# Kernel optimization log

Hardware: AMD Instinct MI355X
Metric: run time of the kernel (lower is better)

The kernel has to match this reference:

```python
import jax, jax.numpy as jnp
import numpy as np

D_MODEL = 512
D_INNER = 1024   # expand=2
D_STATE = 16
D_CONV = 4
DT_RANK = 32     # ceil(d_model/16)
B, L = 2, 2048


def _params(kbase):
    kk = jax.random.split(kbase, 9)
    n = lambda k, s, sc: jax.random.normal(k, s, jnp.float32) * sc
    return dict(
        Win=n(kk[0], (2 * D_INNER, D_MODEL), D_MODEL ** -0.5),
        convw=n(kk[1], (D_INNER, 1, D_CONV), 0.2),
        convb=n(kk[2], (D_INNER,), 0.02),
        Wx=n(kk[3], (DT_RANK + 2 * D_STATE, D_INNER), D_INNER ** -0.5),
        Wdt=n(kk[4], (D_INNER, DT_RANK), DT_RANK ** -0.5),
        dtb=n(kk[5], (D_INNER,), 0.1),
        Alog=n(kk[6], (D_INNER, D_STATE), 0.5),
        Dp=n(kk[7], (D_INNER,), 1.0),
        Wout=n(kk[8], (D_MODEL, D_INNER), D_INNER ** -0.5),
    )


def setup_inputs() -> dict:
    key = jax.random.key(0)
    k0, kf, kr = jax.random.split(key, 3)
    inp = {"hidden_states": jax.random.normal(k0, (B, L, D_MODEL), jnp.float32)}
    for name, v in _params(kf).items():
        inp[name + "_f"] = v
    for name, v in _params(kr).items():
        inp[name + "_r"] = v
    return inp


def _mamba(x, Win, convw, convb, Wx, Wdt, dtb, Alog, Dp, Wout):
    # x: (B, L, D_MODEL)
    Bb = x.shape[0]
    xz = jnp.einsum('bld,ed->ble', x, Win)            # (B, L, 2*D_INNER)
    xs, z = jnp.split(xz, 2, axis=-1)
    # causal depthwise conv over length
    xc = jnp.swapaxes(xs, 1, 2)                       # (B, D_INNER, L)
    xc = jax.lax.conv_general_dilated(
        xc, convw, (1,), [(D_CONV - 1, 0)], feature_group_count=D_INNER)
    xs = jax.nn.silu(jnp.swapaxes(xc + convb[None, :, None], 1, 2))  # (B, L, D_INNER)
    # input-dependent SSM params
    x_dbl = jnp.einsum('bld,ed->ble', xs, Wx)         # (B, L, DT_RANK+2*D_STATE)
    dt = x_dbl[..., :DT_RANK]
    Bm = x_dbl[..., DT_RANK:DT_RANK + D_STATE]        # (B, L, D_STATE)
    Cm = x_dbl[..., DT_RANK + D_STATE:]               # (B, L, D_STATE)
    dt = jax.nn.softplus(jnp.einsum('blr,dr->bld', dt, Wdt) + dtb)   # (B, L, D_INNER)
    A = -jnp.exp(Alog)                                # (D_INNER, D_STATE), strictly negative
    dA = jnp.exp(dt[..., None] * A)                   # (B, L, D_INNER, D_STATE)
    dBu = dt[..., None] * Bm[:, :, None, :] * xs[..., None]

    def step(h, inp):
        dA_t, dBu_t, C_t = inp
        h = dA_t * h + dBu_t                          # (B, D_INNER, D_STATE)
        return h, jnp.einsum('bds,bs->bd', h, C_t)

    h0 = jnp.zeros((Bb, D_INNER, D_STATE), x.dtype)
    _, ys = jax.lax.scan(
        step, h0,
        (jnp.moveaxis(dA, 1, 0), jnp.moveaxis(dBu, 1, 0), jnp.moveaxis(Cm, 1, 0)))
    y = jnp.moveaxis(ys, 0, 1) + xs * Dp              # (B, L, D_INNER)
    y = y * jax.nn.silu(z)                            # gated output
    return jnp.einsum('bld,ed->ble', y, Wout)         # (B, L, D_MODEL)


def reference(hidden_states,
              Win_f, convw_f, convb_f, Wx_f, Wdt_f, dtb_f, Alog_f, Dp_f, Wout_f,
              Win_r, convw_r, convb_r, Wx_r, Wdt_r, dtb_r, Alog_r, Dp_r, Wout_r):
    out_f = _mamba(hidden_states, Win_f, convw_f, convb_f, Wx_f, Wdt_f, dtb_f,
                   Alog_f, Dp_f, Wout_f)
    out_r = _mamba(hidden_states[:, ::-1, :], Win_r, convw_r, convb_r, Wx_r,
                   Wdt_r, dtb_r, Alog_r, Dp_r, Wout_r)[:, ::-1, :]
    return out_f + out_r  # bidirectional_strategy == 'add'
```

## Files before the change

### kernel.cpp

```cpp
#include <hip/hip_runtime.h>
#include <cmath>

#define B_   2
#define L_   2048
#define DM_  512
#define DI_  1024
#define DS_  16
#define DTR_ 32
#define M_   (B_*L_)
#define NC_  64
#define CL_  32
#define KS_  8
#define LOG2E_ 1.44269504088896340736f
#define LN2_   0.69314718055994530942f

typedef __attribute__((ext_vector_type(8))) short short8;
typedef __attribute__((ext_vector_type(4))) float floatx4;

__device__ inline unsigned short f2bf(float f) {
  unsigned u = __float_as_uint(f);
  unsigned r = (u + 0x7fffu + ((u >> 16) & 1u)) >> 16;
  return (unsigned short)r;
}
__device__ inline float bf2f(unsigned short u) {
  return __uint_as_float(((unsigned)u) << 16);
}
__device__ inline unsigned short f2h(float f) {
  _Float16 h = (_Float16)f;
  return *(unsigned short*)&h;
}
__device__ inline float h2f(unsigned short u) {
  _Float16 h = *(_Float16*)&u;
  return (float)h;
}
__device__ inline float fexp2(float x) { return __builtin_amdgcn_exp2f(x); }
__device__ inline float flog2(float x) { return __builtin_amdgcn_logf(x); }

__device__ inline void gload_lds16(const unsigned short* g, unsigned short* l) {
  __builtin_amdgcn_global_load_lds(
      (const __attribute__((address_space(1))) void*)g,
      (__attribute__((address_space(3))) void*)l, 16, 0, 0);
}

__global__ __launch_bounds__(256) void gemm1_mfma_k(
    const unsigned short* __restrict__ A,
    const unsigned short* __restrict__ Wf, const unsigned short* __restrict__ Wr,
    unsigned short* __restrict__ Cf, unsigned short* __restrict__ Cr,
    int M, int N, int K)
{
  __shared__ unsigned short At[128 * 32];
  __shared__ unsigned short Wt[128 * 32];
  const unsigned short* W = blockIdx.z ? Wr : Wf;
  unsigned short* C = blockIdx.z ? Cr : Cf;
  const int tid  = threadIdx.x;
  const int w    = tid >> 6;
  const int lane = tid & 63;
  const int wm   = w >> 1, wn = w & 1;
  const int row0 = blockIdx.y * 128, col0 = blockIdx.x * 128;
  const int lrow  = lane >> 2;
  const int lkoff = (lane & 3) * 8;
  const int fr = lane & 15;
  const int fq = (lane >> 4) * 8;

  floatx4 acc[4][4];
#pragma unroll
  for (int i = 0; i < 4; ++i)
#pragma unroll
    for (int j = 0; j < 4; ++j)
#pragma unroll
      for (int r = 0; r < 4; ++r) acc[i][j][r] = 0.f;

  for (int k0 = 0; k0 < K; k0 += 32) {
#pragma unroll
    for (int j = 0; j < 2; ++j) {
      int r = w * 32 + j * 16;
      gload_lds16(A + (size_t)(row0 + r + lrow) * K + k0 + lkoff, At + r * 32);
      gload_lds16(W + (size_t)(col0 + r + lrow) * K + k0 + lkoff, Wt + r * 32);
    }
    __syncthreads();
    short8 af[4], bf[4];
#pragma unroll
    for (int i = 0; i < 4; ++i) {
      af[i] = *(const short8*)&At[(64 * wm + 16 * i + fr) * 32 + fq];
      bf[i] = *(const short8*)&Wt[(64 * wn + 16 * i + fr) * 32 + fq];
    }
#pragma unroll
    for (int i = 0; i < 4; ++i)
#pragma unroll
      for (int j = 0; j < 4; ++j)
        acc[i][j] = __builtin_amdgcn_mfma_f32_16x16x32_bf16(af[i], bf[j], acc[i][j], 0, 0, 0);
    __syncthreads();
  }
#pragma unroll
  for (int i = 0; i < 4; ++i) {
    int rg = row0 + 64 * wm + 16 * i + ((lane >> 4) << 2);
#pragma unroll
    for (int j = 0; j < 4; ++j) {
      int cg = col0 + 64 * wn + 16 * j + (lane & 15);
#pragma unroll
      for (int r = 0; r < 4; ++r)
        C[(size_t)(rg + r) * N + cg] = f2bf(acc[i][j][r]);
    }
  }
}

__global__ __launch_bounds__(256) void gemm4_fused_k(
    const unsigned short* __restrict__ ybf, const unsigned short* __restrict__ Woutbf,
    const unsigned short* __restrict__ ybr, const unsigned short* __restrict__ Woutbr,
    float* __restrict__ out)
{
  __shared__ unsigned short At[2][64 * 32];
  __shared__ unsigned short Wt[2][64 * 32];
  const int tid  = threadIdx.x;
  const int w    = tid >> 6;
  const int lane = tid & 63;
  const int col0 = blockIdx.x * 64;
  const int row0 = blockIdx.y * 64;
  const int lrow  = lane >> 2;
  const int lkoff = (lane & 3) * 8;
  const int fr = lane & 15;
  const int fq = (lane >> 4) * 8;

  floatx4 acc[4];
#pragma unroll
  for (int j = 0; j < 4; ++j)
#pragma unroll
    for (int r = 0; r < 4; ++r) acc[j][r] = 0.f;

#pragma unroll 1
  for (int src = 0; src < 2; ++src) {
    const unsigned short* A = src ? ybr : ybf;
    const unsigned short* W = src ? Woutbr : Woutbf;
    for (int k0 = 0; k0 < DI_; k0 += 64) {
#pragma unroll
      for (int h = 0; h < 2; ++h) {
        gload_lds16(A + (size_t)(row0 + 16 * w + lrow) * DI_ + k0 + 32 * h + lkoff,
                    At[h] + (16 * w) * 32);
        gload_lds16(W + (size_t)(col0 + 16 * w + lrow) * DI_ + k0 + 32 * h + lkoff,
                    Wt[h] + (16 * w) * 32);
      }
      __syncthreads();
      short8 af[2], bf[2][4];
#pragma unroll
      for (int h = 0; h < 2; ++h) {
        af[h] = *(const short8*)&At[h][(16 * w + fr) * 32 + fq];
#pragma unroll
        for (int j = 0; j < 4; ++j)
          bf[h][j] = *(const short8*)&Wt[h][(16 * j + fr) * 32 + fq];
      }
#pragma unroll
      for (int h = 0; h < 2; ++h)
#pragma unroll
        for (int j = 0; j < 4; ++j)
          acc[j] = __builtin_amdgcn_mfma_f32_16x16x32_bf16(af[h], bf[h][j], acc[j], 0, 0, 0);
      __syncthreads();
    }
  }
  const int rg = row0 + 16 * w + ((lane >> 4) << 2);
#pragma unroll
  for (int j = 0; j < 4; ++j) {
    int cg = col0 + 16 * j + (lane & 15);
#pragma unroll
    for (int r = 0; r < 4; ++r)
      out[(size_t)(rg + r) * DM_ + cg] = acc[j][r];
  }
}

__global__ __launch_bounds__(256) void gemm2_mfma_k(
    const unsigned short* __restrict__ xsbf, const unsigned short* __restrict__ xsbr,
    const unsigned short* __restrict__ Wxbf, const unsigned short* __restrict__ Wxbr,
    float* __restrict__ part)
{
  __shared__ unsigned short At[128 * 32];
  __shared__ unsigned short Wt[64 * 32];
  const int tid  = threadIdx.x;
  const int w    = tid >> 6;
  const int lane = tid & 63;
  const int ks   = blockIdx.x;
  const int row0 = blockIdx.y * 128;
  const int dir  = blockIdx.z;
  const unsigned short* A = dir ? xsbr : xsbf;
  const unsigned short* W = dir ? Wxbr : Wxbf;
  const int kbase = ks * (DI_ / KS_);
  const int lrow  = lane >> 2;
  const int lkoff = (lane & 3) * 8;
  const int fr = lane & 15;
  const int fq = (lane >> 4) * 8;

  floatx4 acc[2][4];
#pragma unroll
  for (int i = 0; i < 2; ++i)
#pragma unroll
    for (int j = 0; j < 4; ++j)
#pragma unroll
      for (int r = 0; r < 4; ++r) acc[i][j][r] = 0.f;

  for (int k0 = 0; k0 < DI_ / KS_; k0 += 32) {
#pragma unroll
    for (int j = 0; j < 2; ++j) {
      int r = w * 32 + j * 16;
      gload_lds16(A + (size_t)(row0 + r + lrow) * DI_ + kbase + k0 + lkoff, At + r * 32);
    }
    {
      int r = w * 16;
      gload_lds16(W + (size_t)(r + lrow) * DI_ + kbase + k0 + lkoff, Wt + r * 32);
    }
    __syncthreads();
    short8 af[2], bf[4];
#pragma unroll
    for (int i = 0; i < 2; ++i)
      af[i] = *(const short8*)&At[(32 * w + 16 * i + fr) * 32 + fq];
#pragma unroll
    for (int j = 0; j < 4; ++j)
      bf[j] = *(const short8*)&Wt[(16 * j + fr) * 32 + fq];
#pragma unroll
    for (int i = 0; i < 2; ++i)
#pragma unroll
      for (int j = 0; j < 4; ++j)
        acc[i][j] = __builtin_amdgcn_mfma_f32_16x16x32_bf16(af[i], bf[j], acc[i][j], 0, 0, 0);
    __syncthreads();
  }
  float* dst = part + (((size_t)dir * KS_ + ks) * M_) * 64;
#pragma unroll
  for (int i = 0; i < 2; ++i) {
    int rg = row0 + 32 * w + 16 * i + ((lane >> 4) << 2);
#pragma unroll
    for (int j = 0; j < 4; ++j) {
      int cg = 16 * j + (lane & 15);
#pragma unroll
      for (int r = 0; r < 4; ++r)
        dst[(size_t)(rg + r) * 64 + cg] = acc[i][j][r];
    }
  }
}

__global__ __launch_bounds__(256) void reduce_part_k(
    const float* __restrict__ part, float* __restrict__ xdf, float* __restrict__ xdr,
    unsigned short* __restrict__ drbf, unsigned short* __restrict__ drbr)
{
  int g = blockIdx.x * 256 + threadIdx.x;
  int n4  = g & 15;
  int m   = (g >> 4) & (M_ - 1);
  int dir = g >> 16;
  const float* p = part + ((size_t)dir * KS_ * M_ + m) * 64 + n4 * 4;
  float4 s = make_float4(0.f, 0.f, 0.f, 0.f);
#pragma unroll
  for (int ks = 0; ks < KS_; ++ks) {
    float4 v = *(const float4*)(p + (size_t)ks * M_ * 64);
    s.x += v.x; s.y += v.y; s.z += v.z; s.w += v.w;
  }
  float* xd = dir ? xdr : xdf;
  *(float4*)(xd + (size_t)m * 64 + n4 * 4) = s;
  if (n4 < 8) {
    unsigned short* dr = dir ? drbr : drbf;
    ushort4 o;
    o.x = f2bf(s.x); o.y = f2bf(s.y); o.z = f2bf(s.z); o.w = f2bf(s.w);
    *(ushort4*)(dr + (size_t)m * 32 + n4 * 4) = o;
  }
}

struct CastArgs {
  const float* src[9];
  unsigned short* dst[9];
  int start[9];
  int n[9];
};

__global__ __launch_bounds__(256) void cast_multi_k(CastArgs a, int total4)
{
  int g = blockIdx.x * 256 + threadIdx.x;
  if (g >= total4) return;
  int e = g * 4;
#pragma unroll 1
  for (int s = 0; s < 9; ++s) {
    if (e < a.start[s] + a.n[s]) {
      int off = e - a.start[s];
      float4 v = *(const float4*)(a.src[s] + off);
      ushort4 o;
      o.x = f2bf(v.x); o.y = f2bf(v.y); o.z = f2bf(v.z); o.w = f2bf(v.w);
      *(ushort4*)(a.dst[s] + off) = o;
      return;
    }
  }
}

__global__ __launch_bounds__(256) void gemm3_mfma_k(
    const unsigned short* __restrict__ drbf, const unsigned short* __restrict__ drbr,
    const unsigned short* __restrict__ Wdtbf, const unsigned short* __restrict__ Wdtbr,
    const float* __restrict__ b0, const float* __restrict__ b1,
    unsigned short* __restrict__ C0, unsigned short* __restrict__ C1)
{
  __shared__ unsigned short At[128 * 32];
  __shared__ unsigned short Wt[128 * 32];
  const unsigned short* A = blockIdx.z ? drbr : drbf;
  const unsigned short* W = blockIdx.z ? Wdtbr : Wdtbf;
  const float* bias = blockIdx.z ? b1 : b0;
  unsigned short* C = blockIdx.z ? C1 : C0;
  const int tid  = threadIdx.x;
  const int w    = tid >> 6;
  const int lane = tid & 63;
  const int wm   = w >> 1, wn = w & 1;
  const int row0 = blockIdx.y * 128, col0 = blockIdx.x * 128;
  const int lrow  = lane >> 2;
  const int lkoff = (lane & 3) * 8;
  const int fr = lane & 15;
  const int fq = (lane >> 4) * 8;

#pragma unroll
  for (int j = 0; j < 2; ++j) {
    int r = w * 32 + j * 16;
    gload_lds16(A + (size_t)(row0 + r + lrow) * DTR_ + lkoff, At + r * 32);
    gload_lds16(W + (size_t)(col0 + r + lrow) * DTR_ + lkoff, Wt + r * 32);
  }
  __syncthreads();
  short8 af[4], bf[4];
#pragma unroll
  for (int i = 0; i < 4; ++i) {
    af[i] = *(const short8*)&At[(64 * wm + 16 * i + fr) * 32 + fq];
    bf[i] = *(const short8*)&Wt[(64 * wn + 16 * i + fr) * 32 + fq];
  }
  floatx4 acc[4][4];
#pragma unroll
  for (int i = 0; i < 4; ++i)
#pragma unroll
    for (int j = 0; j < 4; ++j) {
#pragma unroll
      for (int r = 0; r < 4; ++r) acc[i][j][r] = 0.f;
      acc[i][j] = __builtin_amdgcn_mfma_f32_16x16x32_bf16(af[i], bf[j], acc[i][j], 0, 0, 0);
    }
#pragma unroll
  for (int i = 0; i < 4; ++i) {
    int rg = row0 + 64 * wm + 16 * i + ((lane >> 4) << 2);
#pragma unroll
    for (int j = 0; j < 4; ++j) {
      int cg = col0 + 64 * wn + 16 * j + (lane & 15);
      float bv = bias[cg];
#pragma unroll
      for (int r = 0; r < 4; ++r) {
        float v = acc[i][j][r] + bv;
        float e = fexp2(-fabsf(v) * LOG2E_);
        float sp = fmaxf(v, 0.f) + LN2_ * flog2(1.f + e);
        C[(size_t)(rg + r) * DI_ + cg] = f2h(sp);
      }
    }
  }
}

__global__ __launch_bounds__(256) void conv_silu_k(
    const unsigned short* __restrict__ xzbf, const unsigned short* __restrict__ xzbr,
    const float* __restrict__ cwf, const float* __restrict__ cbf,
    const float* __restrict__ cwr, const float* __restrict__ cbr,
    unsigned short* __restrict__ xsbf, unsigned short* __restrict__ xsbr)
{
  int bid = blockIdx.x;
  int t   = bid & (L_ - 1);
  int b   = (bid >> 11) & (B_ - 1);
  int dir = bid >> 12;
  const unsigned short* xz = dir ? xzbr : xzbf;
  const float* cw = dir ? cwr : cwf;
  const float* cb = dir ? cbr : cbf;
  unsigned short* xsb = dir ? xsbr : xsbf;
  int d0 = threadIdx.x << 2;
  float wv[4][4];
#pragma unroll
  for (int i = 0; i < 4; ++i) {
    float4 w4 = *(const float4*)(cw + (size_t)(d0 + i) * 4);
    wv[i][0] = w4.x; wv[i][1] = w4.y; wv[i][2] = w4.z; wv[i][3] = w4.w;
  }
  float4 cbv = *(const float4*)(cb + d0);
  float acc[4] = {cbv.x, cbv.y, cbv.z, cbv.w};
#pragma unroll
  for (int j = 0; j < 4; ++j) {
    int tt = dir ? (t + 3 - j) : (t - 3 + j);
    if (tt >= 0 && tt < L_) {
      ushort4 v = *(const ushort4*)(xz + ((size_t)b * L_ + tt) * 2048 + d0);
      acc[0] = fmaf(wv[0][j], bf2f(v.x), acc[0]);
      acc[1] = fmaf(wv[1][j], bf2f(v.y), acc[1]);
      acc[2] = fmaf(wv[2][j], bf2f(v.z), acc[2]);
      acc[3] = fmaf(wv[3][j], bf2f(v.w), acc[3]);
    }
  }
  float4 o;
  o.x = acc[0] * __builtin_amdgcn_rcpf(1.f + fexp2(-acc[0] * LOG2E_));
  o.y = acc[1] * __builtin_amdgcn_rcpf(1.f + fexp2(-acc[1] * LOG2E_));
  o.z = acc[2] * __builtin_amdgcn_rcpf(1.f + fexp2(-acc[2] * LOG2E_));
  o.w = acc[3] * __builtin_amdgcn_rcpf(1.f + fexp2(-acc[3] * LOG2E_));
  ushort4 ob;
  ob.x = f2bf(o.x); ob.y = f2bf(o.y); ob.z = f2bf(o.z); ob.w = f2bf(o.w);
  *(ushort4*)(xsb + ((size_t)b * L_ + t) * DI_ + d0) = ob;
}

__global__ __launch_bounds__(256) void scan_passA_k(
    const unsigned short* __restrict__ dtf, const unsigned short* __restrict__ dtr,
    const unsigned short* __restrict__ xsbf, const unsigned short* __restrict__ xsbr,
    const float* __restrict__ xdf, const float* __restrict__ xdr,
    const float* __restrict__ Alogf, const float* __restrict__ Alogr,
    float* __restrict__ E, float* __restrict__ dts)
{
  __shared__ float bS[CL_][16];
  int bid  = blockIdx.x;
  int dgrp = bid & 3;
  int c    = (bid >> 2) & (NC_ - 1);
  int b    = (bid >> 8) & 1;
  int dir  = bid >> 9;
  int d    = (dgrp << 8) + threadIdx.x;
  const unsigned short* dt = dir ? dtr : dtf;
  const unsigned short* xs = dir ? xsbr : xsbf;
  const float* xd = dir ? xdr : xdf;
  const float* Al = dir ? Alogr : Alogf;
  if (threadIdx.x < CL_ * 4) {
    int li = threadIdx.x >> 2;
    int lc = threadIdx.x & 3;
    *(float4*)&bS[li][lc * 4] =
        *(const float4*)(xd + ((size_t)b * L_ + c * CL_ + li) * 64 + 32 + lc * 4);
  }
  float Ai2[16];
#pragma unroll
  for (int s = 0; s < 16; ++s) Ai2[s] = -__expf(Al[(size_t)d * 16 + s]) * LOG2E_;
  float h[16];
#pragma unroll
  for (int s = 0; s < 16; ++s) h[s] = 0.f;
  int t0 = c * CL_ + (dir ? CL_ - 1 : 0);
  const long sdt = (dir ? -1L : 1L) * DI_;
  const unsigned short* dtp = dt + ((size_t)b * L_ + t0) * DI_ + d;
  const unsigned short* xsp = xs + ((size_t)b * L_ + t0) * DI_ + d;
  float dtsum = 0.f;
  __syncthreads();
#pragma unroll 2
  for (int i = 0; i < CL_; ++i) {
    int row = dir ? (CL_ - 1 - i) : i;
    float dtv = h2f(*dtp);
    float xv  = bf2f(*xsp);
    float Bv[16];
#pragma unroll
    for (int q = 0; q < 4; ++q) {
      float4 bq = *(const float4*)&bS[row][4 * q];
      Bv[4*q] = bq.x; Bv[4*q+1] = bq.y; Bv[4*q+2] = bq.z; Bv[4*q+3] = bq.w;
    }
    float dtx = dtv * xv;
    dtsum += dtv;
#pragma unroll
    for (int s = 0; s < 16; ++s) {
      float dA = fexp2(dtv * Ai2[s]);
      h[s] = fmaf(dA, h[s], dtx * Bv[s]);
    }
    dtp += sdt; xsp += sdt;
  }
  size_t base = ((((size_t)dir * B_ + b) * NC_ + c) * DI_ + d) * 16;
#pragma unroll
  for (int q = 0; q < 4; ++q)
    *(float4*)(E + base + q * 4) = make_float4(h[4*q], h[4*q+1], h[4*q+2], h[4*q+3]);
  dts[(((size_t)dir * B_ + b) * NC_ + c) * DI_ + d] = dtsum;
}

__global__ __launch_bounds__(256) void scan_prefix_k(
    const float* __restrict__ E, const float* __restrict__ dts,
    const float* __restrict__ Alogf, const float* __restrict__ Alogr,
    float* __restrict__ Hin)
{
  int gid = blockIdx.x * 256 + threadIdx.x;
  int s   = gid & 15;
  int d   = (gid >> 4) & (DI_ - 1);
  int b   = (gid >> 14) & 1;
  int dir = gid >> 15;
  const float* Al = dir ? Alogr : Alogf;
  float Ai2 = -__expf(Al[(size_t)d * 16 + s]) * LOG2E_;
  size_t eb  = (((size_t)dir * B_ + b) * NC_) * DI_ * 16 + (size_t)d * 16 + s;
  size_t db2 = (((size_t)dir * B_ + b) * NC_) * DI_ + d;
  float h = 0.f;
  if (!dir) {
    for (int c = 0; c < NC_; ++c) {
      size_t idx = eb + (size_t)c * DI_ * 16;
      Hin[idx] = h;
      float Pv = fexp2(dts[db2 + (size_t)c * DI_] * Ai2);
      h = fmaf(Pv, h, E[idx]);
    }
  } else {
    for (int c = NC_ - 1; c >= 0; --c) {
      size_t idx = eb + (size_t)c * DI_ * 16;
      Hin[idx] = h;
      float Pv = fexp2(dts[db2 + (size_t)c * DI_] * Ai2);
      h = fmaf(Pv, h, E[idx]);
    }
  }
}

__global__ __launch_bounds__(256) void scan_passC_k(
    const unsigned short* __restrict__ dtf, const unsigned short* __restrict__ dtr,
    const unsigned short* __restrict__ xsbf, const unsigned short* __restrict__ xsbr,
    const float* __restrict__ xdf, const float* __restrict__ xdr,
    const unsigned short* __restrict__ xzbf, const unsigned short* __restrict__ xzbr,
    const float* __restrict__ Alogf, const float* __restrict__ Alogr,
    const float* __restrict__ Dpf, const float* __restrict__ Dpr,
    const float* __restrict__ Hin,
    unsigned short* __restrict__ ybf, unsigned short* __restrict__ ybr)
{
  __shared__ float bcS[CL_][32];
  int bid  = blockIdx.x;
  int dgrp = bid & 3;
  int c    = (bid >> 2) & (NC_ - 1);
  int b    = (bid >> 8) & 1;
  int dir  = bid >> 9;
  int d    = (dgrp << 8) + threadIdx.x;
  const unsigned short* dt  = dir ? dtr : dtf;
  const unsigned short* xs = dir ? xsbr : xsbf;
  const float* xd  = dir ? xdr : xdf;
  const unsigned short* xz = dir ? xzbr : xzbf;
  const float* Al  = dir ? Alogr : Alogf;
  unsigned short* yb = dir ? ybr : ybf;
  float Dpv = (dir ? Dpr : Dpf)[d];
  {
    int li = threadIdx.x >> 3;
    int lc = threadIdx.x & 7;
    *(float4*)&bcS[li][lc * 4] =
        *(const float4*)(xd + ((size_t)b * L_ + c * CL_ + li) * 64 + 32 + lc * 4);
  }
  float Ai2[16];
#pragma unroll
  for (int s = 0; s < 16; ++s) Ai2[s] = -__expf(Al[(size_t)d * 16 + s]) * LOG2E_;
  size_t hb = ((((size_t)dir * B_ + b) * NC_ + c) * DI_ + d) * 16;
  float h[16];
#pragma unroll
  for (int q = 0; q < 4; ++q) {
    float4 hv = *(const float4*)(Hin + hb + q * 4);
    h[4*q] = hv.x; h[4*q+1] = hv.y; h[4*q+2] = hv.z; h[4*q+3] = hv.w;
  }
  int t0 = c * CL_ + (dir ? CL_ - 1 : 0);
  const long sdt = (dir ? -1L : 1L) * DI_;
  const long sz_ = (dir ? -1L : 1L) * 2048;
  const unsigned short* dtp = dt + ((size_t)b * L_ + t0) * DI_ + d;
  const unsigned short* xsp = xs + ((size_t)b * L_ + t0) * DI_ + d;
  const unsigned short* zp = xz + ((size_t)b * L_ + t0) * 2048 + DI_ + d;
  unsigned short* ybp = yb + ((size_t)b * L_ + t0) * DI_ + d;
  __syncthreads();
#pragma unroll 2
  for (int i = 0; i < CL_; ++i) {
    int row = dir ? (CL_ - 1 - i) : i;
    float dtv = h2f(*dtp);
    float xv  = bf2f(*xsp);
    float z   = bf2f(*zp);
    float Bv[16], Cv[16];
#pragma unroll
    for (int q = 0; q < 4; ++q) {
      float4 bq = *(const float4*)&bcS[row][4 * q];
      float4 cq = *(const float4*)&bcS[row][16 + 4 * q];
      Bv[4*q] = bq.x; Bv[4*q+1] = bq.y; Bv[4*q+2] = bq.z; Bv[4*q+3] = bq.w;
      Cv[4*q] = cq.x; Cv[4*q+1] = cq.y; Cv[4*q+2] = cq.z; Cv[4*q+3] = cq.w;
    }
    float dtx = dtv * xv;
    float yacc = 0.f;
#pragma unroll
    for (int s = 0; s < 16; ++s) {
      float dA = fexp2(dtv * Ai2[s]);
      h[s] = fmaf(dA, h[s], dtx * Bv[s]);
      yacc = fmaf(h[s], Cv[s], yacc);
    }
    float yv = fmaf(xv, Dpv, yacc);
    float sz = z * __builtin_amdgcn_rcpf(1.f + fexp2(-z * LOG2E_));
    *ybp = f2bf(yv * sz);
    dtp += sdt; xsp += sdt; zp += sz_; ybp += sdt;
  }
}

extern "C" void kernel_launch(void* const* d_in, const int* in_sizes, int n_in,
                              void* d_out, int out_size, void* d_ws, size_t ws_size,
                              hipStream_t stream)
{
  const float* x       = (const float*)d_in[0];
  const float* Win_f   = (const float*)d_in[1];
  const float* convw_f = (const float*)d_in[2];
  const float* convb_f = (const float*)d_in[3];
  const float* Wx_f    = (const float*)d_in[4];
  const float* Wdt_f   = (const float*)d_in[5];
  const float* dtb_f   = (const float*)d_in[6];
  const float* Alog_f  = (const float*)d_in[7];
  const float* Dp_f    = (const float*)d_in[8];
  const float* Wout_f  = (const float*)d_in[9];
  const float* Win_r   = (const float*)d_in[10];
  const float* convw_r = (const float*)d_in[11];
  const float* convb_r = (const float*)d_in[12];
  const float* Wx_r    = (const float*)d_in[13];
  const float* Wdt_r   = (const float*)d_in[14];
  const float* dtb_r   = (const float*)d_in[15];
  const float* Alog_r  = (const float*)d_in[16];
  const float* Dp_r    = (const float*)d_in[17];
  const float* Wout_r  = (const float*)d_in[18];
  float* out = (float*)d_out;

  float* ws  = (float*)d_ws;
  float* xdf = ws;
  float* xdr = xdf + (size_t)M_ * 64;
  unsigned short* dtf = (unsigned short*)(xdr + (size_t)M_ * 64);
  unsigned short* dtr = dtf + (size_t)M_ * DI_;
  float* Eb  = (float*)(dtr + (size_t)M_ * DI_);
  float* Hb  = Eb + (size_t)2 * B_ * NC_ * DI_ * 16;
  float* dtsb = Hb + (size_t)2 * B_ * NC_ * DI_ * 16;
  float* part2 = Eb;
  unsigned short* xzbf    = (unsigned short*)(dtsb + (size_t)2 * B_ * NC_ * DI_);
  unsigned short* xzbr    = xzbf + (size_t)M_ * 2048;
  unsigned short* xb      = xzbr + (size_t)M_ * 2048;
  unsigned short* Winb_f  = xb + (size_t)M_ * DM_;
  unsigned short* Winb_r  = Winb_f + (size_t)2048 * DM_;
  unsigned short* Woutb_f = Winb_r + (size_t)2048 * DM_;
  unsigned short* Woutb_r = Woutb_f + (size_t)DM_ * DI_;
  unsigned short* ybf     = Woutb_r + (size_t)DM_ * DI_;
  unsigned short* ybr     = ybf + (size_t)M_ * DI_;
  unsigned short* xsbf    = ybr + (size_t)M_ * DI_;
  unsigned short* xsbr    = xsbf + (size_t)M_ * DI_;
  unsigned short* Wxb_f   = xsbr + (size_t)M_ * DI_;
  unsigned short* Wxb_r   = Wxb_f + (size_t)64 * DI_;
  unsigned short* Wdtb_f  = Wxb_r + (size_t)64 * DI_;
  unsigned short* Wdtb_r  = Wdtb_f + (size_t)DI_ * DTR_;
  unsigned short* drbf    = Wdtb_r + (size_t)DI_ * DTR_;
  unsigned short* drbr    = drbf + (size_t)M_ * DTR_;

  dim3 blk(256);

  {
    CastArgs ca;
    ca.src[0] = x;      ca.dst[0] = xb;      ca.n[0] = M_ * DM_;
    ca.src[1] = Win_f;  ca.dst[1] = Winb_f;  ca.n[1] = 2048 * DM_;
    ca.src[2] = Win_r;  ca.dst[2] = Winb_r;  ca.n[2] = 2048 * DM_;
    ca.src[3] = Wout_f; ca.dst[3] = Woutb_f; ca.n[3] = DM_ * DI_;
    ca.src[4] = Wout_r; ca.dst[4] = Woutb_r; ca.n[4] = DM_ * DI_;
    ca.src[5] = Wx_f;   ca.dst[5] = Wxb_f;   ca.n[5] = 64 * DI_;
    ca.src[6] = Wx_r;   ca.dst[6] = Wxb_r;   ca.n[6] = 64 * DI_;
    ca.src[7] = Wdt_f;  ca.dst[7] = Wdtb_f;  ca.n[7] = DI_ * DTR_;
    ca.src[8] = Wdt_r;  ca.dst[8] = Wdtb_r;  ca.n[8] = DI_ * DTR_;
    int st = 0;
    for (int s = 0; s < 9; ++s) { ca.start[s] = st; st += ca.n[s]; }
    int total4 = st / 4;
    cast_multi_k<<<(total4 + 255) / 256, blk, 0, stream>>>(ca, total4);
  }

  gemm1_mfma_k<<<dim3(2048 / 128, M_ / 128, 2), blk, 0, stream>>>(
      xb, Winb_f, Winb_r, xzbf, xzbr, M_, 2048, DM_);

  conv_silu_k<<<2 * B_ * L_, blk, 0, stream>>>(xzbf, xzbr, convw_f, convb_f,
      convw_r, convb_r, xsbf, xsbr);

  gemm2_mfma_k<<<dim3(KS_, M_ / 128, 2), blk, 0, stream>>>(
      xsbf, xsbr, Wxb_f, Wxb_r, part2);
  reduce_part_k<<<(2 * M_ * 16) / 256, blk, 0, stream>>>(part2, xdf, xdr,
      drbf, drbr);

  gemm3_mfma_k<<<dim3(DI_ / 128, M_ / 128, 2), blk, 0, stream>>>(
      drbf, drbr, Wdtb_f, Wdtb_r, dtb_f, dtb_r, dtf, dtr);

  scan_passA_k<<<2 * B_ * NC_ * 4, blk, 0, stream>>>(dtf, dtr, xsbf, xsbr,
      xdf, xdr, Alog_f, Alog_r, Eb, dtsb);
  scan_prefix_k<<<(2 * B_ * DI_ * 16) / 256, blk, 0, stream>>>(
      Eb, dtsb, Alog_f, Alog_r, Hb);
  scan_passC_k<<<2 * B_ * NC_ * 4, blk, 0, stream>>>(dtf, dtr, xsbf, xsbr,
      xdf, xdr, xzbf, xzbr, Alog_f, Alog_r, Dp_f, Dp_r, Hb, ybf, ybr);

  gemm4_fused_k<<<dim3(DM_ / 64, M_ / 64), blk, 0, stream>>>(
      ybf, Woutb_f, ybr, Woutb_r, out);
}
```

Baseline: 270.5 us.

## Double-buffer GEMM LDS tiles, precompute A table, software-pipeline scan prefix loads

The MFMA GEMM kernels (gemm1, gemm2, gemm4) now use double-buffered LDS tiles, so the next K-tile's global-to-LDS load is issued before computing the current one, and only one barrier is needed per iteration. The -exp(Alog)*log2e table is computed once in the cast kernel and read with float4 loads by the scan kernels instead of being recomputed per thread. The scan prefix loop preloads the next chunk's E and dt values to hide load latency. The cost is doubled shared memory per block, which may lower occupancy, plus a small extra buffer in the workspace.

```diff
diff --git a/kernel.cpp b/kernel.cpp
--- a/kernel.cpp
+++ b/kernel.cpp
@@ -48,8 +48,8 @@
     unsigned short* __restrict__ Cf, unsigned short* __restrict__ Cr,
     int M, int N, int K)
 {
-  __shared__ unsigned short At[128 * 32];
-  __shared__ unsigned short Wt[128 * 32];
+  __shared__ unsigned short At[2][128 * 32];
+  __shared__ unsigned short Wt[2][128 * 32];
   const unsigned short* W = blockIdx.z ? Wr : Wf;
   unsigned short* C = blockIdx.z ? Cr : Cf;
   const int tid  = threadIdx.x;
@@ -70,27 +70,40 @@
 #pragma unroll
       for (int r = 0; r < 4; ++r) acc[i][j][r] = 0.f;
 
-  for (int k0 = 0; k0 < K; k0 += 32) {
+  auto stage = [&](int buf, int k0) {
 #pragma unroll
     for (int j = 0; j < 2; ++j) {
       int r = w * 32 + j * 16;
-      gload_lds16(A + (size_t)(row0 + r + lrow) * K + k0 + lkoff, At + r * 32);
-      gload_lds16(W + (size_t)(col0 + r + lrow) * K + k0 + lkoff, Wt + r * 32);
-    }
-    __syncthreads();
+      gload_lds16(A + (size_t)(row0 + r + lrow) * K + k0 + lkoff, At[buf] + r * 32);
+      gload_lds16(W + (size_t)(col0 + r + lrow) * K + k0 + lkoff, Wt[buf] + r * 32);
+    }
+  };
+  auto compute = [&](int buf) {
     short8 af[4], bf[4];
 #pragma unroll
     for (int i = 0; i < 4; ++i) {
-      af[i] = *(const short8*)&At[(64 * wm + 16 * i + fr) * 32 + fq];
-      bf[i] = *(const short8*)&Wt[(64 * wn + 16 * i + fr) * 32 + fq];
+      af[i] = *(const short8*)&At[buf][(64 * wm + 16 * i + fr) * 32 + fq];
+      bf[i] = *(const short8*)&Wt[buf][(64 * wn + 16 * i + fr) * 32 + fq];
     }
 #pragma unroll
     for (int i = 0; i < 4; ++i)
 #pragma unroll
       for (int j = 0; j < 4; ++j)
         acc[i][j] = __builtin_amdgcn_mfma_f32_16x16x32_bf16(af[i], bf[j], acc[i][j], 0, 0, 0);
+  };
+
+  const int NT = K >> 5;
+  stage(0, 0);
+  __syncthreads();
+  int cur = 0;
+  for (int t = 0; t < NT - 1; ++t) {
+    stage(cur ^ 1, (t + 1) << 5);
+    compute(cur);
     __syncthreads();
-  }
+    cur ^= 1;
+  }
+  compute(cur);
+
 #pragma unroll
   for (int i = 0; i < 4; ++i) {
     int rg = row0 + 64 * wm + 16 * i + ((lane >> 4) << 2);
@@ -109,8 +122,8 @@
     const unsigned short* __restrict__ ybr, const unsigned short* __restrict__ Woutbr,
     float* __restrict__ out)
 {
-  __shared__ unsigned short At[2][64 * 32];
-  __shared__ unsigned short Wt[2][64 * 32];
+  __shared__ unsigned short At[2][2][64 * 32];
+  __shared__ unsigned short Wt[2][2][64 * 32];
   const int tid  = threadIdx.x;
   const int w    = tid >> 6;
   const int lane = tid & 63;
@@ -127,35 +140,45 @@
 #pragma unroll
     for (int r = 0; r < 4; ++r) acc[j][r] = 0.f;
 
-#pragma unroll 1
-  for (int src = 0; src < 2; ++src) {
-    const unsigned short* A = src ? ybr : ybf;
-    const unsigned short* W = src ? Woutbr : Woutbf;
-    for (int k0 = 0; k0 < DI_; k0 += 64) {
-#pragma unroll
-      for (int h = 0; h < 2; ++h) {
-        gload_lds16(A + (size_t)(row0 + 16 * w + lrow) * DI_ + k0 + 32 * h + lkoff,
-                    At[h] + (16 * w) * 32);
-        gload_lds16(W + (size_t)(col0 + 16 * w + lrow) * DI_ + k0 + 32 * h + lkoff,
-                    Wt[h] + (16 * w) * 32);
-      }
-      __syncthreads();
-      short8 af[2], bf[2][4];
-#pragma unroll
-      for (int h = 0; h < 2; ++h) {
-        af[h] = *(const short8*)&At[h][(16 * w + fr) * 32 + fq];
-#pragma unroll
-        for (int j = 0; j < 4; ++j)
-          bf[h][j] = *(const short8*)&Wt[h][(16 * j + fr) * 32 + fq];
-      }
-#pragma unroll
-      for (int h = 0; h < 2; ++h)
-#pragma unroll
-        for (int j = 0; j < 4; ++j)
-          acc[j] = __builtin_amdgcn_mfma_f32_16x16x32_bf16(af[h], bf[h][j], acc[j], 0, 0, 0);
-      __syncthreads();
-    }
-  }
+  auto stage = [&](int buf, int t) {
+    const unsigned short* A = (t & 16) ? ybr : ybf;
+    const unsigned short* W = (t & 16) ? Woutbr : Woutbf;
+    const int k0 = (t & 15) << 6;
+#pragma unroll
+    for (int h = 0; h < 2; ++h) {
+      gload_lds16(A + (size_t)(row0 + 16 * w + lrow) * DI_ + k0 + 32 * h + lkoff,
+                  At[buf][h] + (16 * w) * 32);
+      gload_lds16(W + (size_t)(col0 + 16 * w + lrow) * DI_ + k0 + 32 * h + lkoff,
+                  Wt[buf][h] + (16 * w) * 32);
+    }
+  };
+  auto compute = [&](int buf) {
+    short8 af[2], bf[2][4];
+#pragma unroll
+    for (int h = 0; h < 2; ++h) {
+      af[h] = *(const short8*)&At[buf][h][(16 * w + fr) * 32 + fq];
+#pragma unroll
+      for (int j = 0; j < 4; ++j)
+        bf[h][j] = *(const short8*)&Wt[buf][h][(16 * j + fr) * 32 + fq];
+    }
+#pragma unroll
+    for (int h = 0; h < 2; ++h)
+#pragma unroll
+      for (int j = 0; j < 4; ++j)
+        acc[j] = __builtin_amdgcn_mfma_f32_16x16x32_bf16(af[h], bf[h][j], acc[j], 0, 0, 0);
+  };
+
+  stage(0, 0);
+  __syncthreads();
+  int cur = 0;
+  for (int t = 0; t < 31; ++t) {
+    stage(cur ^ 1, t + 1);
+    compute(cur);
+    __syncthreads();
+    cur ^= 1;
+  }
+  compute(cur);
+
   const int rg = row0 + 16 * w + ((lane >> 4) << 2);
 #pragma unroll
   for (int j = 0; j < 4; ++j) {
@@ -171,8 +194,8 @@
     const unsigned short* __restrict__ Wxbf, const unsigned short* __restrict__ Wxbr,
     float* __restrict__ part)
 {
-  __shared__ unsigned short At[128 * 32];
-  __shared__ unsigned short Wt[64 * 32];
+  __shared__ unsigned short At[2][128 * 32];
+  __shared__ unsigned short Wt[2][64 * 32];
   const int tid  = threadIdx.x;
   const int w    = tid >> 6;
   const int lane = tid & 63;
@@ -195,31 +218,42 @@
 #pragma unroll
       for (int r = 0; r < 4; ++r) acc[i][j][r] = 0.f;
 
-  for (int k0 = 0; k0 < DI_ / KS_; k0 += 32) {
+  auto stage = [&](int buf, int k0) {
 #pragma unroll
     for (int j = 0; j < 2; ++j) {
       int r = w * 32 + j * 16;
-      gload_lds16(A + (size_t)(row0 + r + lrow) * DI_ + kbase + k0 + lkoff, At + r * 32);
-    }
-    {
-      int r = w * 16;
-      gload_lds16(W + (size_t)(r + lrow) * DI_ + kbase + k0 + lkoff, Wt + r * 32);
-    }
-    __syncthreads();
+      gload_lds16(A + (size_t)(row0 + r + lrow) * DI_ + kbase + k0 + lkoff, At[buf] + r * 32);
+    }
+    int r = w * 16;
+    gload_lds16(W + (size_t)(r + lrow) * DI_ + kbase + k0 + lkoff, Wt[buf] + r * 32);
+  };
+  auto compute = [&](int buf) {
     short8 af[2], bf[4];
 #pragma unroll
     for (int i = 0; i < 2; ++i)
-      af[i] = *(const short8*)&At[(32 * w + 16 * i + fr) * 32 + fq];
+      af[i] = *(const short8*)&At[buf][(32 * w + 16 * i + fr) * 32 + fq];
 #pragma unroll
     for (int j = 0; j < 4; ++j)
-      bf[j] = *(const short8*)&Wt[(16 * j + fr) * 32 + fq];
+      bf[j] = *(const short8*)&Wt[buf][(16 * j + fr) * 32 + fq];
 #pragma unroll
     for (int i = 0; i < 2; ++i)
 #pragma unroll
       for (int j = 0; j < 4; ++j)
         acc[i][j] = __builtin_amdgcn_mfma_f32_16x16x32_bf16(af[i], bf[j], acc[i][j], 0, 0, 0);
+  };
+
+  const int NT = (DI_ / KS_) >> 5;
+  stage(0, 0);
+  __syncthreads();
+  int cur = 0;
+  for (int t = 0; t < NT - 1; ++t) {
+    stage(cur ^ 1, (t + 1) << 5);
+    compute(cur);
     __syncthreads();
-  }
+    cur ^= 1;
+  }
+  compute(cur);
+
   float* dst = part + (((size_t)dir * KS_ + ks) * M_) * 64;
 #pragma unroll
   for (int i = 0; i < 2; ++i) {
@@ -266,10 +300,22 @@
   int n[9];
 };
 
-__global__ __launch_bounds__(256) void cast_multi_k(CastArgs a, int total4)
+__global__ __launch_bounds__(256) void cast_multi_k(
+    CastArgs a, int total4,
+    const float* __restrict__ Alf, const float* __restrict__ Alr,
+    float* __restrict__ Atf, float* __restrict__ Atr)
 {
   int g = blockIdx.x * 256 + threadIdx.x;
   if (g >= total4) return;
+  if (g < 8192) {
+    const float* Al = (g < 4096) ? Alf : Alr;
+    float* At = (g < 4096) ? Atf : Atr;
+    int off = (g & 4095) * 4;
+    float4 v = *(const float4*)(Al + off);
+    float4 o = make_float4(-__expf(v.x) * LOG2E_, -__expf(v.y) * LOG2E_,
+                           -__expf(v.z) * LOG2E_, -__expf(v.w) * LOG2E_);
+    *(float4*)(At + off) = o;
+  }
   int e = g * 4;
 #pragma unroll 1
   for (int s = 0; s < 9; ++s) {
@@ -394,7 +440,7 @@
     const unsigned short* __restrict__ dtf, const unsigned short* __restrict__ dtr,
     const unsigned short* __restrict__ xsbf, const unsigned short* __restrict__ xsbr,
     const float* __restrict__ xdf, const float* __restrict__ xdr,
-    const float* __restrict__ Alogf, const float* __restrict__ Alogr,
+    const float* __restrict__ Atabf, const float* __restrict__ Atabr,
     float* __restrict__ E, float* __restrict__ dts)
 {
   __shared__ float bS[CL_][16];
@@ -407,7 +453,7 @@
   const unsigned short* dt = dir ? dtr : dtf;
   const unsigned short* xs = dir ? xsbr : xsbf;
   const float* xd = dir ? xdr : xdf;
-  const float* Al = dir ? Alogr : Alogf;
+  const float* At = dir ? Atabr : Atabf;
   if (threadIdx.x < CL_ * 4) {
     int li = threadIdx.x >> 2;
     int lc = threadIdx.x & 3;
@@ -416,7 +462,10 @@
   }
   float Ai2[16];
 #pragma unroll
-  for (int s = 0; s < 16; ++s) Ai2[s] = -__expf(Al[(size_t)d * 16 + s]) * LOG2E_;
+  for (int q = 0; q < 4; ++q) {
+    float4 a4 = *(const float4*)(At + (size_t)d * 16 + q * 4);
+    Ai2[4*q] = a4.x; Ai2[4*q+1] = a4.y; Ai2[4*q+2] = a4.z; Ai2[4*q+3] = a4.w;
+  }
   float h[16];
 #pragma unroll
   for (int s = 0; s < 16; ++s) h[s] = 0.f;
@@ -455,7 +504,7 @@
 
 __global__ __launch_bounds__(256) void scan_prefix_k(
     const float* __restrict__ E, const float* __restrict__ dts,
-    const float* __restrict__ Alogf, const float* __restrict__ Alogr,
+    const float* __restrict__ Atabf, const float* __restrict__ Atabr,
     float* __restrict__ Hin)
 {
   int gid = blockIdx.x * 256 + threadIdx.x;
@@ -463,25 +512,37 @@
   int d   = (gid >> 4) & (DI_ - 1);
   int b   = (gid >> 14) & 1;
   int dir = gid >> 15;
-  const float* Al = dir ? Alogr : Alogf;
-  float Ai2 = -__expf(Al[(size_t)d * 16 + s]) * LOG2E_;
+  float Ai2 = (dir ? Atabr : Atabf)[(size_t)d * 16 + s];
   size_t eb  = (((size_t)dir * B_ + b) * NC_) * DI_ * 16 + (size_t)d * 16 + s;
   size_t db2 = (((size_t)dir * B_ + b) * NC_) * DI_ + d;
+  const long es = (long)DI_ * 16;
   float h = 0.f;
   if (!dir) {
-    for (int c = 0; c < NC_; ++c) {
-      size_t idx = eb + (size_t)c * DI_ * 16;
+    size_t idx = eb;
+    size_t di  = db2;
+    float Ec = E[idx], dc = dts[di];
+#pragma unroll 2
+    for (int c = 0; c < NC_ - 1; ++c) {
+      float En = E[idx + es];
+      float dn = dts[di + DI_];
       Hin[idx] = h;
-      float Pv = fexp2(dts[db2 + (size_t)c * DI_] * Ai2);
-      h = fmaf(Pv, h, E[idx]);
-    }
+      h = fmaf(fexp2(dc * Ai2), h, Ec);
+      Ec = En; dc = dn; idx += es; di += DI_;
+    }
+    Hin[idx] = h;
   } else {
-    for (int c = NC_ - 1; c >= 0; --c) {
-      size_t idx = eb + (size_t)c * DI_ * 16;
+    size_t idx = eb + (size_t)(NC_ - 1) * es;
+    size_t di  = db2 + (size_t)(NC_ - 1) * DI_;
+    float Ec = E[idx], dc = dts[di];
+#pragma unroll 2
+    for (int c = 0; c < NC_ - 1; ++c) {
+      float En = E[idx - es];
+      float dn = dts[di - DI_];
       Hin[idx] = h;
-      float Pv = fexp2(dts[db2 + (size_t)c * DI_] * Ai2);
-      h = fmaf(Pv, h, E[idx]);
-    }
+      h = fmaf(fexp2(dc * Ai2), h, Ec);
+      Ec = En; dc = dn; idx -= es; di -= DI_;
+    }
+    Hin[idx] = h;
   }
 }
 
@@ -490,7 +551,7 @@
     const unsigned short* __restrict__ xsbf, const unsigned short* __restrict__ xsbr,
     const float* __restrict__ xdf, const float* __restrict__ xdr,
     const unsigned short* __restrict__ xzbf, const unsigned short* __restrict__ xzbr,
-    const float* __restrict__ Alogf, const float* __restrict__ Alogr,
+    const float* __restrict__ Atabf, const float* __restrict__ Atabr,
     const float* __restrict__ Dpf, const float* __restrict__ Dpr,
     const float* __restrict__ Hin,
     unsigned short* __restrict__ ybf, unsigned short* __restrict__ ybr)
@@ -506,7 +567,7 @@
   const unsigned short* xs = dir ? xsbr : xsbf;
   const float* xd  = dir ? xdr : xdf;
   const unsigned short* xz = dir ? xzbr : xzbf;
-  const float* Al  = dir ? Alogr : Alogf;
+  const float* At  = dir ? Atabr : Atabf;
   unsigned short* yb = dir ? ybr : ybf;
   float Dpv = (dir ? Dpr : Dpf)[d];
   {
@@ -517,7 +578,10 @@
   }
   float Ai2[16];
 #pragma unroll
-  for (int s = 0; s < 16; ++s) Ai2[s] = -__expf(Al[(size_t)d * 16 + s]) * LOG2E_;
+  for (int q = 0; q < 4; ++q) {
+    float4 a4 = *(const float4*)(At + (size_t)d * 16 + q * 4);
+    Ai2[4*q] = a4.x; Ai2[4*q+1] = a4.y; Ai2[4*q+2] = a4.z; Ai2[4*q+3] = a4.w;
+  }
   size_t hb = ((((size_t)dir * B_ + b) * NC_ + c) * DI_ + d) * 16;
   float h[16];
 #pragma unroll
@@ -613,6 +677,8 @@
   unsigned short* Wdtb_r  = Wdtb_f + (size_t)DI_ * DTR_;
   unsigned short* drbf    = Wdtb_r + (size_t)DI_ * DTR_;
   unsigned short* drbr    = drbf + (size_t)M_ * DTR_;
+  float* Atabf = (float*)(drbr + (size_t)M_ * DTR_);
+  float* Atabr = Atabf + (size_t)DI_ * DS_;
 
   dim3 blk(256);
 
@@ -630,7 +696,8 @@
     int st = 0;
     for (int s = 0; s < 9; ++s) { ca.start[s] = st; st += ca.n[s]; }
     int total4 = st / 4;
-    cast_multi_k<<<(total4 + 255) / 256, blk, 0, stream>>>(ca, total4);
+    cast_multi_k<<<(total4 + 255) / 256, blk, 0, stream>>>(
+        ca, total4, Alog_f, Alog_r, Atabf, Atabr);
   }
 
   gemm1_mfma_k<<<dim3(2048 / 128, M_ / 128, 2), blk, 0, stream>>>(
@@ -648,11 +715,11 @@
       drbf, drbr, Wdtb_f, Wdtb_r, dtb_f, dtb_r, dtf, dtr);
 
   scan_passA_k<<<2 * B_ * NC_ * 4, blk, 0, stream>>>(dtf, dtr, xsbf, xsbr,
-      xdf, xdr, Alog_f, Alog_r, Eb, dtsb);
+      xdf, xdr, Atabf, Atabr, Eb, dtsb);
   scan_prefix_k<<<(2 * B_ * DI_ * 16) / 256, blk, 0, stream>>>(
-      Eb, dtsb, Alog_f, Alog_r, Hb);
+      Eb, dtsb, Atabf, Atabr, Hb);
   scan_passC_k<<<2 * B_ * NC_ * 4, blk, 0, stream>>>(dtf, dtr, xsbf, xsbr,
-      xdf, xdr, xzbf, xzbr, Alog_f, Alog_r, Dp_f, Dp_r, Hb, ybf, ybr);
+      xdf, xdr, xzbf, xzbr, Atabf, Atabr, Dp_f, Dp_r, Hb, ybf, ybr);
 
   gemm4_fused_k<<<dim3(DM_ / 64, M_ / 64), blk, 0, stream>>>(
       ybf, Woutb_f, ybr, Woutb_r, out);
```

Result: no change. 272.3 us (+0.7%).
